# Kernel optimization log

Measured on AMD Instinct MI355X. Metric: run time of the kernel, lower is better.

## Reference

```python
import jax, jax.numpy as jnp
import numpy as np

B, S, IN_DIM, OUT_DIM, G = 8, 2048, 512, 256, 8
CHUNK = 128  # positions per scan step; per-chunk phi = CHUNK*O*O*G floats
EPS = 1e-5   # torch LayerNorm default


def make_periods():
    # periods[i,j,g] = i*(O*G) + j*G + g + 2
    i = jnp.arange(OUT_DIM, dtype=jnp.float32)[:, None, None]
    j = jnp.arange(OUT_DIM, dtype=jnp.float32)[None, :, None]
    g = jnp.arange(G, dtype=jnp.float32)[None, None, :]
    return i * (OUT_DIM * G) + j * G + g + 2.0


def setup_inputs() -> dict:
    key = jax.random.key(0)
    ks = jax.random.split(key, 4)
    x = jax.random.normal(ks[0], (B, S, IN_DIM), dtype=jnp.float32)
    positions = jnp.arange(S, dtype=jnp.int64 if jax.config.jax_enable_x64 else jnp.int32)
    M = jax.random.uniform(ks[1], (OUT_DIM, IN_DIM), minval=-0.5, maxval=0.5, dtype=jnp.float32)
    P = jax.random.uniform(ks[2], (OUT_DIM, OUT_DIM, G), minval=-0.1, maxval=0.1, dtype=jnp.float32)
    W_res = jax.random.uniform(ks[3], (OUT_DIM, IN_DIM), minval=-0.1, maxval=0.1, dtype=jnp.float32)
    ln_scale = jnp.ones((OUT_DIM,), dtype=jnp.float32)
    ln_bias = jnp.zeros((OUT_DIM,), dtype=jnp.float32)
    periods = make_periods()
    return {"x": x, "M": M, "P": P, "W_res": W_res, "ln_scale": ln_scale,
            "ln_bias": ln_bias, "periods": periods, "positions": positions}


def layer_norm(h, scale, bias):
    mu = jnp.mean(h, axis=-1, keepdims=True)
    var = jnp.mean(jnp.square(h - mu), axis=-1, keepdims=True)  # biased, like torch
    return (h - mu) * jax.lax.rsqrt(var + EPS) * scale + bias


def reference(x, M, P, W_res, ln_scale, ln_bias, periods, positions):
    # x: (B,S,in), M: (out,in), P: (out,out,G), periods: (out,out,G)
    x_trans = layer_norm(jnp.einsum('bsi,oi->bso', x, M), ln_scale, ln_bias)

    two_pi = jnp.float32(2.0 * np.pi)
    pos_chunks = positions.astype(jnp.float32).reshape(-1, CHUNK)  # (S/CHUNK, CHUNK)

    def body(carry, pos):
        # phi: (CHUNK, O, O, G); reduce over g first to avoid the huge 5D tensor
        phi = jnp.cos(two_pi * pos[:, None, None, None] / periods)
        A = jnp.einsum('sijg,ijg->sij', phi, P)  # (CHUNK, O, O)
        return carry, A

    _, A = jax.lax.scan(body, 0, pos_chunks)
    A = A.reshape(S, OUT_DIM, OUT_DIM)  # A[s,i,j] = sum_g P[i,j,g]*cos(2*pi*k_s/T_ijg)

    Nk = jnp.einsum('bsj,sij->bsi', x_trans, A)  # (B,S,out)
    residual = jnp.einsum('bsi,oi->bso', x, W_res)  # separate residual proj
    return Nk + residual
```

## Files before the change

### kernel.cpp

```cpp
#include <hip/hip_runtime.h>
#include <hip/hip_bf16.h>
#include <math.h>

#define B_   8
#define S_   2048
#define IN_  512
#define OUT_ 256
#define G_   8


typedef float  f32x4  __attribute__((ext_vector_type(4)));
typedef short  s16x8  __attribute__((ext_vector_type(8)));
typedef __bf16 bf16x8 __attribute__((ext_vector_type(8)));
typedef unsigned short u16x8 __attribute__((ext_vector_type(8)));

__device__ __forceinline__ float cos2pi(float f) {
#if __has_builtin(__builtin_amdgcn_cosf)
    return __builtin_amdgcn_cosf(f);
#else
    return __cosf(6.28318530717958647692f * f);
#endif
}

__device__ __forceinline__ float fractf_(float f) {
#if __has_builtin(__builtin_amdgcn_fractf)
    return __builtin_amdgcn_fractf(f);
#else
    return f - floorf(f);
#endif
}

__device__ __forceinline__ unsigned short f2bf(float f) {
    unsigned u = __builtin_bit_cast(unsigned, f);
    u += 0x7fffu + ((u >> 16) & 1u);
    return (unsigned short)(u >> 16);
}

template <typename T>
__device__ __forceinline__ auto mfma_bf16_(T a, T b, f32x4 c, int)
    -> decltype(__builtin_amdgcn_mfma_f32_16x16x32_bf16(a, b, c, 0, 0, 0)) {
    return __builtin_amdgcn_mfma_f32_16x16x32_bf16(a, b, c, 0, 0, 0);
}
template <typename T>
__device__ __forceinline__ auto mfma_bf16_(T a, T b, f32x4 c, long)
    -> decltype(__builtin_amdgcn_mfma_f32_16x16x32_bf16(__builtin_bit_cast(bf16x8, a),
                                                        __builtin_bit_cast(bf16x8, b), c, 0, 0, 0)) {
    return __builtin_amdgcn_mfma_f32_16x16x32_bf16(__builtin_bit_cast(bf16x8, a),
                                                   __builtin_bit_cast(bf16x8, b), c, 0, 0, 0);
}
__device__ __forceinline__ f32x4 mfma_bf16(s16x8 a, s16x8 b, f32x4 c) {
    return mfma_bf16_(a, b, c, 0);
}

__device__ __forceinline__ void gld16(const void* g, void* l) {
    __builtin_amdgcn_global_load_lds((const __attribute__((address_space(1))) unsigned int*)g,
                                     (__attribute__((address_space(3))) unsigned int*)l,
                                     16, 0, 0);
}

__global__ __launch_bounds__(256) void cvt_x(const float* __restrict__ x,
                                             unsigned short* __restrict__ Xb) {
    const int idx = blockIdx.x * 256 + threadIdx.x;
    const float4 v0 = *(const float4*)(x + (size_t)idx * 8);
    const float4 v1 = *(const float4*)(x + (size_t)idx * 8 + 4);
    u16x8 o;
    o[0] = f2bf(v0.x); o[1] = f2bf(v0.y); o[2] = f2bf(v0.z); o[3] = f2bf(v0.w);
    o[4] = f2bf(v1.x); o[5] = f2bf(v1.y); o[6] = f2bf(v1.z); o[7] = f2bf(v1.w);
    *(u16x8*)(Xb + (size_t)idx * 8) = o;
}

__global__ __launch_bounds__(256) void cvt_w(const float* __restrict__ M,
                                             const float* __restrict__ Wres,
                                             unsigned short* __restrict__ Wb) {
    const int idx = blockIdx.x * 256 + threadIdx.x;
    const int row = idx >> 6;
    const int col = (idx & 63) * 8;
    const float* src = (row < 256) ? (M + (size_t)row * 512 + col)
                                   : (Wres + (size_t)(row - 256) * 512 + col);
    const float4 v0 = *(const float4*)(src);
    const float4 v1 = *(const float4*)(src + 4);
    u16x8 o;
    o[0] = f2bf(v0.x); o[1] = f2bf(v0.y); o[2] = f2bf(v0.z); o[3] = f2bf(v0.w);
    o[4] = f2bf(v1.x); o[5] = f2bf(v1.y); o[6] = f2bf(v1.z); o[7] = f2bf(v1.w);
    *(u16x8*)(Wb + (size_t)row * 512 + col) = o;
}

__global__ __launch_bounds__(256) void gemm_mfma(const unsigned short* __restrict__ Xb,
                                                 const unsigned short* __restrict__ Wb,
                                                 float* __restrict__ y,
                                                 float* __restrict__ out) {
    __shared__ __align__(16) unsigned short At[128 * 64];
    __shared__ __align__(16) unsigned short Bt[128 * 64];
    const int t    = threadIdx.x;
    const int col0 = blockIdx.x * 128;
    const int row0 = blockIdx.y * 128;

    const unsigned short* ga[4];
    const unsigned short* gb[4];
    int lofs[4];
#pragma unroll
    for (int cc = 0; cc < 4; ++cc) {
        const int L = cc * 256 + t;
        const int r = L >> 3;
        const int c = (L & 7) ^ (r & 7);
        ga[cc]   = Xb + (size_t)(row0 + r) * 512 + c * 8;
        gb[cc]   = Wb + (size_t)(col0 + r) * 512 + c * 8;
        lofs[cc] = L * 8;
    }

    const int lane = t & 63;
    const int wave = t >> 6;
    const int wm   = (wave & 1) * 64;
    const int wn   = (wave >> 1) * 64;
    const int quad = lane >> 4;
    const int l16  = lane & 15;

    f32x4 acc[4][4];
#pragma unroll
    for (int mi = 0; mi < 4; ++mi)
#pragma unroll
        for (int ni = 0; ni < 4; ++ni) acc[mi][ni] = {0.0f, 0.0f, 0.0f, 0.0f};

    for (int k0 = 0; k0 < 512; k0 += 64) {
        __syncthreads();
#pragma unroll
        for (int cc = 0; cc < 4; ++cc) {
            gld16(ga[cc] + k0, At + lofs[cc]);
            gld16(gb[cc] + k0, Bt + lofs[cc]);
        }
        __syncthreads();
#pragma unroll
        for (int ks = 0; ks < 2; ++ks) {
            s16x8 af[4], bf[4];
#pragma unroll
            for (int mi = 0; mi < 4; ++mi) {
                const int cc = (ks * 4 + quad) ^ (l16 & 7);
                const int ra = wm + mi * 16 + l16;
                const int rb = wn + mi * 16 + l16;
                af[mi] = *(const s16x8*)(At + (ra * 8 + cc) * 8);
                bf[mi] = *(const s16x8*)(Bt + (rb * 8 + cc) * 8);
            }
#pragma unroll
            for (int mi = 0; mi < 4; ++mi)
#pragma unroll
                for (int ni = 0; ni < 4; ++ni)
                    acc[mi][ni] = mfma_bf16(af[mi], bf[ni], acc[mi][ni]);
        }
    }

    float* dst   = (col0 < 256) ? y : out;
    const int cb = (col0 & 255) + wn;
#pragma unroll
    for (int mi = 0; mi < 4; ++mi) {
        const int rbase = row0 + wm + mi * 16 + quad * 4;
#pragma unroll
        for (int ni = 0; ni < 4; ++ni) {
            const int col = cb + ni * 16 + l16;
#pragma unroll
            for (int rg = 0; rg < 4; ++rg)
                dst[(size_t)(rbase + rg) * 256 + col] = acc[mi][ni][rg];
        }
    }
}

__global__ __launch_bounds__(256) void gemm_kernel(const float* __restrict__ x,
                                                   const float* __restrict__ M,
                                                   const float* __restrict__ Wres,
                                                   float* __restrict__ y,
                                                   float* __restrict__ out) {
    __shared__ float As[8][132];
    __shared__ float Bs[8][132];
    const int ct = blockIdx.x;
    const int rt = blockIdx.y;
    const int t  = threadIdx.x;
    const int row0 = rt * 128;
    const float* W = (ct < 2) ? M : Wres;
    const int wcol0 = (ct & 1) * 128;
    float acc[8][8];
#pragma unroll
    for (int r = 0; r < 8; ++r)
#pragma unroll
        for (int c = 0; c < 8; ++c) acc[r][c] = 0.0f;
    const int lr = t >> 1;
    const int lk = (t & 1) << 2;
    for (int k0 = 0; k0 < 512; k0 += 8) {
        float4 av = *(const float4*)(x + (size_t)(row0 + lr) * 512 + k0 + lk);
        float4 bv = *(const float4*)(W + (size_t)(wcol0 + lr) * 512 + k0 + lk);
        __syncthreads();
        As[lk + 0][lr] = av.x; As[lk + 1][lr] = av.y; As[lk + 2][lr] = av.z; As[lk + 3][lr] = av.w;
        Bs[lk + 0][lr] = bv.x; Bs[lk + 1][lr] = bv.y; Bs[lk + 2][lr] = bv.z; Bs[lk + 3][lr] = bv.w;
        __syncthreads();
        const int tx = t & 15, ty = t >> 4;
#pragma unroll
        for (int kk = 0; kk < 8; ++kk) {
            const float4 a0 = *(const float4*)&As[kk][ty * 8];
            const float4 a1 = *(const float4*)&As[kk][ty * 8 + 4];
            const float4 b0 = *(const float4*)&Bs[kk][tx * 8];
            const float4 b1 = *(const float4*)&Bs[kk][tx * 8 + 4];
            const float ar[8] = {a0.x, a0.y, a0.z, a0.w, a1.x, a1.y, a1.z, a1.w};
            const float br[8] = {b0.x, b0.y, b0.z, b0.w, b1.x, b1.y, b1.z, b1.w};
#pragma unroll
            for (int r = 0; r < 8; ++r)
#pragma unroll
                for (int c = 0; c < 8; ++c) acc[r][c] = fmaf(ar[r], br[c], acc[r][c]);
        }
    }
    const int tx = t & 15, ty = t >> 4;
    float* dst = (ct < 2) ? y : out;
    const int cbase = (ct & 1) * 128 + tx * 8;
#pragma unroll
    for (int r = 0; r < 8; ++r) {
        float4 v0 = {acc[r][0], acc[r][1], acc[r][2], acc[r][3]};
        float4 v1 = {acc[r][4], acc[r][5], acc[r][6], acc[r][7]};
        float* p = dst + (size_t)(row0 + ty * 8 + r) * 256 + cbase;
        *(float4*)(p)     = v0;
        *(float4*)(p + 4) = v1;
    }
}

__global__ __launch_bounds__(256) void ln_kernel(float* __restrict__ y,
                                                 const float* __restrict__ scale,
                                                 const float* __restrict__ bias) {
    const int t    = threadIdx.x;
    const int row  = blockIdx.x * 4 + (t >> 6);
    const int lane = t & 63;
    float* p = y + (size_t)row * 256 + lane * 4;
    float4 v = *(float4*)p;
    float s  = v.x + v.y + v.z + v.w;
    float ss = v.x * v.x + v.y * v.y + v.z * v.z + v.w * v.w;
#pragma unroll
    for (int off = 32; off > 0; off >>= 1) {
        s  += __shfl_xor(s, off);
        ss += __shfl_xor(ss, off);
    }
    const float mu  = s * (1.0f / 256.0f);
    const float var = ss * (1.0f / 256.0f) - mu * mu;
    const float rs  = rsqrtf(var + 1e-5f);
    float4 sc = *(const float4*)(scale + lane * 4);
    float4 bi = *(const float4*)(bias + lane * 4);
    float4 o;
    o.x = (v.x - mu) * rs * sc.x + bi.x;
    o.y = (v.y - mu) * rs * sc.y + bi.y;
    o.z = (v.z - mu) * rs * sc.z + bi.z;
    o.w = (v.w - mu) * rs * sc.w + bi.w;
    *(float4*)p = o;
}

__global__ __launch_bounds__(256) void prep_ptk(const float* __restrict__ P,
                                                const float* __restrict__ periods,
                                                float4* __restrict__ PTK) {
    const int tid = blockIdx.x * 256 + threadIdx.x;
    const int j = tid >> 8, i = tid & 255;
    float p[8], iT[8], k2[8];
#pragma unroll
    for (int g = 0; g < 8; ++g) {
        const int idx = (i * 256 + j) * 8 + g;
        p[g]  = P[idx];
        iT[g] = 1.0f / periods[idx];
        k2[g] = 2.0f * cos2pi(iT[g]);
    }
    float4* base = PTK + (size_t)(j * 6) * 256 + i;
    base[0]    = make_float4(p[0], iT[0], p[1], iT[1]);
    base[256]  = make_float4(p[2], iT[2], p[3], iT[3]);
    base[512]  = make_float4(p[4], iT[4], p[5], iT[5]);
    base[768]  = make_float4(p[6], iT[6], p[7], iT[7]);
    base[1024] = make_float4(k2[0], k2[1], k2[2], k2[3]);
    base[1280] = make_float4(k2[4], k2[5], k2[6], k2[7]);
}

__global__ __launch_bounds__(256, 2) void cosnk8(const float4* __restrict__ PTK,
                                                 const float* __restrict__ xt,
                                                 float* __restrict__ out) {
    __shared__ float xs[256][64];
    const int t  = threadIdx.x;
    const int bx = blockIdx.x;
    const int ih = (bx >> 2) & 1;
    const int stile = ((bx >> 3) << 2) | (bx & 3);
    const int s0 = stile * 8;

    {
        const int slot = t >> 2;
        const int st   = slot >> 3;
        const int b    = slot & 7;
        const int jb   = (t & 3) * 64;
        const float* src = xt + (size_t)(b * S_ + s0 + st) * 256 + jb;
#pragma unroll
        for (int q = 0; q < 16; ++q) {
            float4 v = *(const float4*)(src + 4 * q);
            xs[jb + 4 * q + 0][slot] = v.x;
            xs[jb + 4 * q + 1][slot] = v.y;
            xs[jb + 4 * q + 2][slot] = v.z;
            xs[jb + 4 * q + 3][slot] = v.w;
        }
    }
    __syncthreads();

    const int i  = ih * 128 + (t & 127);
    const int jh = t >> 7;
    const int j0 = jh * 128;
    const float sv0 = (float)s0;

    float acc[8][8];
#pragma unroll
    for (int s = 0; s < 8; ++s)
#pragma unroll
        for (int b = 0; b < 8; ++b) acc[s][b] = 0.0f;

    const float4* ptk = PTK + (size_t)(j0 * 6) * 256 + i;
    float4 q0 = ptk[0],    q1 = ptk[256],  q2 = ptk[512];
    float4 q3 = ptk[768], k01 = ptk[1024], k23 = ptk[1280];

#define CHEB8(p_, iT_, k2_)                         \
    do {                                            \
        float f0 = fractf_(sv0 * (iT_));            \
        float c0 = cos2pi(f0);                      \
        float c1 = cos2pi(fractf_(f0 + (iT_)));     \
        float c2 = fmaf((k2_), c1, -c0);            \
        float c3 = fmaf((k2_), c2, -c1);            \
        float c4 = fmaf((k2_), c3, -c2);            \
        float c5 = fmaf((k2_), c4, -c3);            \
        float c6 = fmaf((k2_), c5, -c4);            \
        float c7 = fmaf((k2_), c6, -c5);            \
        a0 = fmaf((p_), c0, a0); a1 = fmaf((p_), c1, a1); \
        a2 = fmaf((p_), c2, a2); a3 = fmaf((p_), c3, a3); \
        a4 = fmaf((p_), c4, a4); a5 = fmaf((p_), c5, a5); \
        a6 = fmaf((p_), c6, a6); a7 = fmaf((p_), c7, a7); \
    } while (0)

    for (int jj = 0; jj < 128; ++jj) {
        const float4* pn = ptk + ((jj < 127) ? 1536 : 0);
        const float4 n0 = pn[0],   n1 = pn[256],  n2 = pn[512];
        const float4 n3 = pn[768], n4 = pn[1024], n5 = pn[1280];

        float a0 = 0.f, a1 = 0.f, a2 = 0.f, a3 = 0.f, a4 = 0.f, a5 = 0.f, a6 = 0.f, a7 = 0.f;
        CHEB8(q0.x, q0.y, k01.x);
        CHEB8(q0.z, q0.w, k01.y);
        CHEB8(q1.x, q1.y, k01.z);
        CHEB8(q1.z, q1.w, k01.w);
        CHEB8(q2.x, q2.y, k23.x);
        CHEB8(q2.z, q2.w, k23.y);
        CHEB8(q3.x, q3.y, k23.z);
        CHEB8(q3.z, q3.w, k23.w);

        const float* xrow = &xs[j0 + jj][0];
        const float as_[8] = {a0, a1, a2, a3, a4, a5, a6, a7};
#pragma unroll
        for (int s = 0; s < 8; ++s) {
            const float4 xa = *(const float4*)(xrow + s * 8);
            const float4 xb = *(const float4*)(xrow + s * 8 + 4);
            acc[s][0] = fmaf(as_[s], xa.x, acc[s][0]);
            acc[s][1] = fmaf(as_[s], xa.y, acc[s][1]);
            acc[s][2] = fmaf(as_[s], xa.z, acc[s][2]);
            acc[s][3] = fmaf(as_[s], xa.w, acc[s][3]);
            acc[s][4] = fmaf(as_[s], xb.x, acc[s][4]);
            acc[s][5] = fmaf(as_[s], xb.y, acc[s][5]);
            acc[s][6] = fmaf(as_[s], xb.z, acc[s][6]);
            acc[s][7] = fmaf(as_[s], xb.w, acc[s][7]);
        }
        q0 = n0; q1 = n1; q2 = n2; q3 = n3; k01 = n4; k23 = n5;
        ptk = pn;
    }
#undef CHEB8

    __syncthreads();
    float* red = &xs[0][0];
    const int tl = t & 127;
    if (jh) {
#pragma unroll
        for (int slot = 0; slot < 64; ++slot)
            red[slot * 128 + tl] = acc[slot >> 3][slot & 7];
    }
    __syncthreads();
    if (!jh) {
#pragma unroll
        for (int slot = 0; slot < 64; ++slot) {
            const int st = slot >> 3, b = slot & 7;
            const float v = acc[st][b] + red[slot * 128 + tl];
            out[(size_t)(b * S_ + s0 + st) * 256 + i] += v;
        }
    }
}

extern "C" void kernel_launch(void* const* d_in, const int* in_sizes, int n_in,
                              void* d_out, int out_size, void* d_ws, size_t ws_size,
                              hipStream_t stream) {
    const float* x        = (const float*)d_in[0];
    const float* M        = (const float*)d_in[1];
    const float* P        = (const float*)d_in[2];
    const float* Wres     = (const float*)d_in[3];
    const float* ln_scale = (const float*)d_in[4];
    const float* ln_bias  = (const float*)d_in[5];
    const float* periods  = (const float*)d_in[6];

    float* out = (float*)d_out;
    char*  wsb = (char*)d_ws;
    float* y   = (float*)wsb;
    unsigned short* Xb = (unsigned short*)(wsb + (size_t)16 * 1024 * 1024);
    float4* PTK        = (float4*)(wsb + (size_t)16 * 1024 * 1024);
    unsigned short* Wb = (unsigned short*)(wsb + (size_t)32 * 1024 * 1024);

    const bool use_mfma = (ws_size >= (size_t)34078720);

    if (use_mfma) {
        cvt_x<<<4096, 256, 0, stream>>>(x, Xb);
        cvt_w<<<128, 256, 0, stream>>>(M, Wres, Wb);
        dim3 ggrid(4, 128);
        gemm_mfma<<<ggrid, 256, 0, stream>>>(Xb, Wb, y, out);
    } else {
        dim3 ggrid(4, 128);
        gemm_kernel<<<ggrid, 256, 0, stream>>>(x, M, Wres, y, out);
    }

    ln_kernel<<<4096, 256, 0, stream>>>(y, ln_scale, ln_bias);

    prep_ptk<<<256, 256, 0, stream>>>(P, periods, PTK);

    cosnk8<<<512, 256, 0, stream>>>(PTK, y, out);
}
```

Before: 235.5 us.

## Use fp16 dot2 for cos-weighted contraction, shrink GEMM tile, merge conversion kernels

```diff
diff --git a/kernel.cpp b/kernel.cpp
--- a/kernel.cpp
+++ b/kernel.cpp
@@ -9,10 +9,12 @@
 #define G_   8
 
 
-typedef float  f32x4  __attribute__((ext_vector_type(4)));
-typedef short  s16x8  __attribute__((ext_vector_type(8)));
-typedef __bf16 bf16x8 __attribute__((ext_vector_type(8)));
+typedef float    f32x4  __attribute__((ext_vector_type(4)));
+typedef short    s16x8  __attribute__((ext_vector_type(8)));
+typedef __bf16   bf16x8 __attribute__((ext_vector_type(8)));
 typedef unsigned short u16x8 __attribute__((ext_vector_type(8)));
+typedef _Float16 h2     __attribute__((ext_vector_type(2)));
+typedef _Float16 h16x8  __attribute__((ext_vector_type(8)));
 
 __device__ __forceinline__ float cos2pi(float f) {
 #if __has_builtin(__builtin_amdgcn_cosf)
@@ -36,6 +38,37 @@
     return (unsigned short)(u >> 16);
 }
 
+__device__ __forceinline__ h2 pkrtz2(float a, float b) {
+#if __has_builtin(__builtin_amdgcn_cvt_pkrtz)
+    return __builtin_bit_cast(h2, __builtin_amdgcn_cvt_pkrtz(a, b));
+#else
+    h2 r; r[0] = (_Float16)a; r[1] = (_Float16)b; return r;
+#endif
+}
+
+#if __has_builtin(__builtin_amdgcn_fdot2)
+template <typename T>
+__device__ __forceinline__ auto fdot2_impl(T a, T b, float c, int)
+    -> decltype(__builtin_amdgcn_fdot2(a, b, c, false)) {
+    return __builtin_amdgcn_fdot2(a, b, c, false);
+}
+typedef __fp16 fp16v2 __attribute__((ext_vector_type(2)));
+template <typename T>
+__device__ __forceinline__ auto fdot2_impl(T a, T b, float c, long)
+    -> decltype(__builtin_amdgcn_fdot2(__builtin_bit_cast(fp16v2, a),
+                                       __builtin_bit_cast(fp16v2, b), c, false)) {
+    return __builtin_amdgcn_fdot2(__builtin_bit_cast(fp16v2, a),
+                                  __builtin_bit_cast(fp16v2, b), c, false);
+}
+__device__ __forceinline__ float fdot2_(h2 a, h2 b, float c) {
+    return fdot2_impl(a, b, c, 0);
+}
+#else
+__device__ __forceinline__ float fdot2_(h2 a, h2 b, float c) {
+    return c + (float)a[0] * (float)b[0] + (float)a[1] * (float)b[1];
+}
+#endif
+
 template <typename T>
 __device__ __forceinline__ auto mfma_bf16_(T a, T b, f32x4 c, int)
     -> decltype(__builtin_amdgcn_mfma_f32_16x16x32_bf16(a, b, c, 0, 0, 0)) {
@@ -58,92 +91,100 @@
                                      16, 0, 0);
 }
 
-__global__ __launch_bounds__(256) void cvt_x(const float* __restrict__ x,
-                                             unsigned short* __restrict__ Xb) {
-    const int idx = blockIdx.x * 256 + threadIdx.x;
-    const float4 v0 = *(const float4*)(x + (size_t)idx * 8);
-    const float4 v1 = *(const float4*)(x + (size_t)idx * 8 + 4);
-    u16x8 o;
-    o[0] = f2bf(v0.x); o[1] = f2bf(v0.y); o[2] = f2bf(v0.z); o[3] = f2bf(v0.w);
-    o[4] = f2bf(v1.x); o[5] = f2bf(v1.y); o[6] = f2bf(v1.z); o[7] = f2bf(v1.w);
-    *(u16x8*)(Xb + (size_t)idx * 8) = o;
-}
-
-__global__ __launch_bounds__(256) void cvt_w(const float* __restrict__ M,
-                                             const float* __restrict__ Wres,
-                                             unsigned short* __restrict__ Wb) {
-    const int idx = blockIdx.x * 256 + threadIdx.x;
-    const int row = idx >> 6;
-    const int col = (idx & 63) * 8;
-    const float* src = (row < 256) ? (M + (size_t)row * 512 + col)
-                                   : (Wres + (size_t)(row - 256) * 512 + col);
+__global__ __launch_bounds__(256) void cvt_xw(const float* __restrict__ x,
+                                              const float* __restrict__ M,
+                                              const float* __restrict__ Wres,
+                                              unsigned short* __restrict__ Xb,
+                                              unsigned short* __restrict__ Wb) {
+    const int bid = blockIdx.x;
+    const float* src;
+    unsigned short* dst;
+    if (bid < 4096) {
+        const int idx = bid * 256 + threadIdx.x;
+        src = x + (size_t)idx * 8;
+        dst = Xb + (size_t)idx * 8;
+    } else {
+        const int idx = (bid - 4096) * 256 + threadIdx.x;
+        const int row = idx >> 6;
+        const int col = (idx & 63) * 8;
+        src = (row < 256) ? (M + (size_t)row * 512 + col)
+                          : (Wres + (size_t)(row - 256) * 512 + col);
+        dst = Wb + (size_t)row * 512 + col;
+    }
     const float4 v0 = *(const float4*)(src);
     const float4 v1 = *(const float4*)(src + 4);
     u16x8 o;
     o[0] = f2bf(v0.x); o[1] = f2bf(v0.y); o[2] = f2bf(v0.z); o[3] = f2bf(v0.w);
     o[4] = f2bf(v1.x); o[5] = f2bf(v1.y); o[6] = f2bf(v1.z); o[7] = f2bf(v1.w);
-    *(u16x8*)(Wb + (size_t)row * 512 + col) = o;
+    *(u16x8*)dst = o;
 }
 
 __global__ __launch_bounds__(256) void gemm_mfma(const unsigned short* __restrict__ Xb,
                                                  const unsigned short* __restrict__ Wb,
                                                  float* __restrict__ y,
                                                  float* __restrict__ out) {
-    __shared__ __align__(16) unsigned short At[128 * 64];
+    __shared__ __align__(16) unsigned short At[64 * 64];
     __shared__ __align__(16) unsigned short Bt[128 * 64];
     const int t    = threadIdx.x;
     const int col0 = blockIdx.x * 128;
-    const int row0 = blockIdx.y * 128;
-
-    const unsigned short* ga[4];
-    const unsigned short* gb[4];
-    int lofs[4];
+    const int row0 = blockIdx.y * 64;
+
+    const unsigned short* ga[2]; int la[2];
+    const unsigned short* gb[4]; int lb[4];
+#pragma unroll
+    for (int cc = 0; cc < 2; ++cc) {
+        const int L = cc * 256 + t;
+        const int r = L >> 3;
+        const int c = (L & 7) ^ (r & 7);
+        ga[cc] = Xb + (size_t)(row0 + r) * 512 + c * 8;
+        la[cc] = L * 8;
+    }
 #pragma unroll
     for (int cc = 0; cc < 4; ++cc) {
         const int L = cc * 256 + t;
         const int r = L >> 3;
         const int c = (L & 7) ^ (r & 7);
-        ga[cc]   = Xb + (size_t)(row0 + r) * 512 + c * 8;
-        gb[cc]   = Wb + (size_t)(col0 + r) * 512 + c * 8;
-        lofs[cc] = L * 8;
+        gb[cc] = Wb + (size_t)(col0 + r) * 512 + c * 8;
+        lb[cc] = L * 8;
     }
 
     const int lane = t & 63;
     const int wave = t >> 6;
-    const int wm   = (wave & 1) * 64;
-    const int wn   = (wave >> 1) * 64;
+    const int wn   = wave * 32;
     const int quad = lane >> 4;
     const int l16  = lane & 15;
 
-    f32x4 acc[4][4];
+    f32x4 acc[4][2];
 #pragma unroll
     for (int mi = 0; mi < 4; ++mi)
 #pragma unroll
-        for (int ni = 0; ni < 4; ++ni) acc[mi][ni] = {0.0f, 0.0f, 0.0f, 0.0f};
+        for (int ni = 0; ni < 2; ++ni) acc[mi][ni] = {0.0f, 0.0f, 0.0f, 0.0f};
 
     for (int k0 = 0; k0 < 512; k0 += 64) {
         __syncthreads();
 #pragma unroll
-        for (int cc = 0; cc < 4; ++cc) {
-            gld16(ga[cc] + k0, At + lofs[cc]);
-            gld16(gb[cc] + k0, Bt + lofs[cc]);
-        }
+        for (int cc = 0; cc < 2; ++cc) gld16(ga[cc] + k0, At + la[cc]);
+#pragma unroll
+        for (int cc = 0; cc < 4; ++cc) gld16(gb[cc] + k0, Bt + lb[cc]);
         __syncthreads();
 #pragma unroll
         for (int ks = 0; ks < 2; ++ks) {
-            s16x8 af[4], bf[4];
+            const int cc = (ks * 4 + quad) ^ (l16 & 7);
+            s16x8 af[4], bf[2];
 #pragma unroll
             for (int mi = 0; mi < 4; ++mi) {
-                const int cc = (ks * 4 + quad) ^ (l16 & 7);
-                const int ra = wm + mi * 16 + l16;
-                const int rb = wn + mi * 16 + l16;
+                const int ra = mi * 16 + l16;
                 af[mi] = *(const s16x8*)(At + (ra * 8 + cc) * 8);
-                bf[mi] = *(const s16x8*)(Bt + (rb * 8 + cc) * 8);
             }
 #pragma unroll
+            for (int ni = 0; ni < 2; ++ni) {
+                const int rb = wn + ni * 16 + l16;
+                bf[ni] = *(const s16x8*)(Bt + (rb * 8 + cc) * 8);
+            }
+#pragma unroll
             for (int mi = 0; mi < 4; ++mi)
 #pragma unroll
-                for (int ni = 0; ni < 4; ++ni)
+                for (int ni = 0; ni < 2; ++ni)
                     acc[mi][ni] = mfma_bf16(af[mi], bf[ni], acc[mi][ni]);
         }
     }
@@ -152,9 +193,9 @@
     const int cb = (col0 & 255) + wn;
 #pragma unroll
     for (int mi = 0; mi < 4; ++mi) {
-        const int rbase = row0 + wm + mi * 16 + quad * 4;
-#pragma unroll
-        for (int ni = 0; ni < 4; ++ni) {
+        const int rbase = row0 + mi * 16 + quad * 4;
+#pragma unroll
+        for (int ni = 0; ni < 2; ++ni) {
             const int col = cb + ni * 16 + l16;
 #pragma unroll
             for (int rg = 0; rg < 4; ++rg)
@@ -268,10 +309,13 @@
     base[1280] = make_float4(k2[4], k2[5], k2[6], k2[7]);
 }
 
-__global__ __launch_bounds__(256, 2) void cosnk8(const float4* __restrict__ PTK,
-                                                 const float* __restrict__ xt,
-                                                 float* __restrict__ out) {
-    __shared__ float xs[256][64];
+__global__ __launch_bounds__(256, 4) void cosnk_dot(const float4* __restrict__ PTK,
+                                                    const float* __restrict__ xt,
+                                                    float* __restrict__ out) {
+    __shared__ __align__(16) char smem[32768];
+    h2*    xsh = (h2*)smem;
+    float* red = (float*)smem;
+
     const int t  = threadIdx.x;
     const int bx = blockIdx.x;
     const int ih = (bx >> 2) & 1;
@@ -282,15 +326,14 @@
         const int slot = t >> 2;
         const int st   = slot >> 3;
         const int b    = slot & 7;
-        const int jb   = (t & 3) * 64;
-        const float* src = xt + (size_t)(b * S_ + s0 + st) * 256 + jb;
+        const int jg   = t & 3;
+        const float* src = xt + (size_t)(b * S_ + s0 + st) * 256 + jg * 64;
 #pragma unroll
         for (int q = 0; q < 16; ++q) {
             float4 v = *(const float4*)(src + 4 * q);
-            xs[jb + 4 * q + 0][slot] = v.x;
-            xs[jb + 4 * q + 1][slot] = v.y;
-            xs[jb + 4 * q + 2][slot] = v.z;
-            xs[jb + 4 * q + 3][slot] = v.w;
+            const int jp = jg * 32 + 2 * q;
+            xsh[(jp + 0) * 64 + slot] = pkrtz2(v.x, v.y);
+            xsh[(jp + 1) * 64 + slot] = pkrtz2(v.z, v.w);
         }
     }
     __syncthreads();
@@ -298,6 +341,7 @@
     const int i  = ih * 128 + (t & 127);
     const int jh = t >> 7;
     const int j0 = jh * 128;
+    const int jpb = jh * 64;
     const float sv0 = (float)s0;
 
     float acc[8][8];
@@ -307,10 +351,8 @@
         for (int b = 0; b < 8; ++b) acc[s][b] = 0.0f;
 
     const float4* ptk = PTK + (size_t)(j0 * 6) * 256 + i;
-    float4 q0 = ptk[0],    q1 = ptk[256],  q2 = ptk[512];
-    float4 q3 = ptk[768], k01 = ptk[1024], k23 = ptk[1280];
-
-#define CHEB8(p_, iT_, k2_)                         \
+
+#define CHEB8(p_, iT_, k2_, A)                      \
     do {                                            \
         float f0 = fractf_(sv0 * (iT_));            \
         float c0 = cos2pi(f0);                      \
@@ -321,49 +363,60 @@
         float c5 = fmaf((k2_), c4, -c3);            \
         float c6 = fmaf((k2_), c5, -c4);            \
         float c7 = fmaf((k2_), c6, -c5);            \
-        a0 = fmaf((p_), c0, a0); a1 = fmaf((p_), c1, a1); \
-        a2 = fmaf((p_), c2, a2); a3 = fmaf((p_), c3, a3); \
-        a4 = fmaf((p_), c4, a4); a5 = fmaf((p_), c5, a5); \
-        a6 = fmaf((p_), c6, a6); a7 = fmaf((p_), c7, a7); \
+        A[0] = fmaf((p_), c0, A[0]); A[1] = fmaf((p_), c1, A[1]); \
+        A[2] = fmaf((p_), c2, A[2]); A[3] = fmaf((p_), c3, A[3]); \
+        A[4] = fmaf((p_), c4, A[4]); A[5] = fmaf((p_), c5, A[5]); \
+        A[6] = fmaf((p_), c6, A[6]); A[7] = fmaf((p_), c7, A[7]); \
     } while (0)
 
-    for (int jj = 0; jj < 128; ++jj) {
-        const float4* pn = ptk + ((jj < 127) ? 1536 : 0);
-        const float4 n0 = pn[0],   n1 = pn[256],  n2 = pn[512];
-        const float4 n3 = pn[768], n4 = pn[1024], n5 = pn[1280];
-
-        float a0 = 0.f, a1 = 0.f, a2 = 0.f, a3 = 0.f, a4 = 0.f, a5 = 0.f, a6 = 0.f, a7 = 0.f;
-        CHEB8(q0.x, q0.y, k01.x);
-        CHEB8(q0.z, q0.w, k01.y);
-        CHEB8(q1.x, q1.y, k01.z);
-        CHEB8(q1.z, q1.w, k01.w);
-        CHEB8(q2.x, q2.y, k23.x);
-        CHEB8(q2.z, q2.w, k23.y);
-        CHEB8(q3.x, q3.y, k23.z);
-        CHEB8(q3.z, q3.w, k23.w);
-
-        const float* xrow = &xs[j0 + jj][0];
-        const float as_[8] = {a0, a1, a2, a3, a4, a5, a6, a7};
+    for (int jj = 0; jj < 64; ++jj) {
+        float e[8] = {0.f, 0.f, 0.f, 0.f, 0.f, 0.f, 0.f, 0.f};
+        {
+            const float4 q0 = ptk[0],   q1  = ptk[256],  q2  = ptk[512];
+            const float4 q3 = ptk[768], k01 = ptk[1024], k23 = ptk[1280];
+            CHEB8(q0.x, q0.y, k01.x, e);
+            CHEB8(q0.z, q0.w, k01.y, e);
+            CHEB8(q1.x, q1.y, k01.z, e);
+            CHEB8(q1.z, q1.w, k01.w, e);
+            CHEB8(q2.x, q2.y, k23.x, e);
+            CHEB8(q2.z, q2.w, k23.y, e);
+            CHEB8(q3.x, q3.y, k23.z, e);
+            CHEB8(q3.z, q3.w, k23.w, e);
+        }
+        float o[8] = {0.f, 0.f, 0.f, 0.f, 0.f, 0.f, 0.f, 0.f};
+        {
+            const float4 q0 = ptk[1536], q1  = ptk[1792], q2  = ptk[2048];
+            const float4 q3 = ptk[2304], k01 = ptk[2560], k23 = ptk[2816];
+            CHEB8(q0.x, q0.y, k01.x, o);
+            CHEB8(q0.z, q0.w, k01.y, o);
+            CHEB8(q1.x, q1.y, k01.z, o);
+            CHEB8(q1.z, q1.w, k01.w, o);
+            CHEB8(q2.x, q2.y, k23.x, o);
+            CHEB8(q2.z, q2.w, k23.y, o);
+            CHEB8(q3.x, q3.y, k23.z, o);
+            CHEB8(q3.z, q3.w, k23.w, o);
+        }
+        ptk += 3072;
+
+        const h2* xrow = xsh + (size_t)(jpb + jj) * 64;
 #pragma unroll
         for (int s = 0; s < 8; ++s) {
-            const float4 xa = *(const float4*)(xrow + s * 8);
-            const float4 xb = *(const float4*)(xrow + s * 8 + 4);
-            acc[s][0] = fmaf(as_[s], xa.x, acc[s][0]);
-            acc[s][1] = fmaf(as_[s], xa.y, acc[s][1]);
-            acc[s][2] = fmaf(as_[s], xa.z, acc[s][2]);
-            acc[s][3] = fmaf(as_[s], xa.w, acc[s][3]);
-            acc[s][4] = fmaf(as_[s], xb.x, acc[s][4]);
-            acc[s][5] = fmaf(as_[s], xb.y, acc[s][5]);
-            acc[s][6] = fmaf(as_[s], xb.z, acc[s][6]);
-            acc[s][7] = fmaf(as_[s], xb.w, acc[s][7]);
-        }
-        q0 = n0; q1 = n1; q2 = n2; q3 = n3; k01 = n4; k23 = n5;
-        ptk = pn;
+            const h2 ap = pkrtz2(e[s], o[s]);
+            const h16x8 hx0 = *(const h16x8*)(xrow + s * 8);
+            const h16x8 hx1 = *(const h16x8*)(xrow + s * 8 + 4);
+            acc[s][0] = fdot2_(ap, __builtin_shufflevector(hx0, hx0, 0, 1), acc[s][0]);
+            acc[s][1] = fdot2_(ap, __builtin_shufflevector(hx0, hx0, 2, 3), acc[s][1]);
+            acc[s][2] = fdot2_(ap, __builtin_shufflevector(hx0, hx0, 4, 5), acc[s][2]);
+            acc[s][3] = fdot2_(ap, __builtin_shufflevector(hx0, hx0, 6, 7), acc[s][3]);
+            acc[s][4] = fdot2_(ap, __builtin_shufflevector(hx1, hx1, 0, 1), acc[s][4]);
+            acc[s][5] = fdot2_(ap, __builtin_shufflevector(hx1, hx1, 2, 3), acc[s][5]);
+            acc[s][6] = fdot2_(ap, __builtin_shufflevector(hx1, hx1, 4, 5), acc[s][6]);
+            acc[s][7] = fdot2_(ap, __builtin_shufflevector(hx1, hx1, 6, 7), acc[s][7]);
+        }
     }
 #undef CHEB8
 
     __syncthreads();
-    float* red = &xs[0][0];
     const int tl = t & 127;
     if (jh) {
 #pragma unroll
@@ -402,9 +455,8 @@
     const bool use_mfma = (ws_size >= (size_t)34078720);
 
     if (use_mfma) {
-        cvt_x<<<4096, 256, 0, stream>>>(x, Xb);
-        cvt_w<<<128, 256, 0, stream>>>(M, Wres, Wb);
-        dim3 ggrid(4, 128);
+        cvt_xw<<<4224, 256, 0, stream>>>(x, M, Wres, Xb, Wb);
+        dim3 ggrid(4, 256);
         gemm_mfma<<<ggrid, 256, 0, stream>>>(Xb, Wb, y, out);
     } else {
         dim3 ggrid(4, 128);
@@ -415,5 +467,5 @@
 
     prep_ptk<<<256, 256, 0, stream>>>(P, periods, PTK);
 
-    cosnk8<<<512, 256, 0, stream>>>(PTK, y, out);
-}
+    cosnk_dot<<<512, 256, 0, stream>>>(PTK, y, out);
+}
```

Measured after the change: 271.6 us. 1.15x slower.
